# Optimization experiments

Measured on AMD Instinct MI355X. Metric: run time of the kernel, lower is better.

The kernel has to match this reference:

```python
import jax, jax.numpy as jnp
import numpy as np

N = 20000        # number of graph nodes (objects + regions)
E = 660000       # number of directed edges (~avg degree 33)
F_DIM = 254      # feature_dims = in_feats // 2
IN_FEATS = 508   # (256 - 2) * 2
GLOVE = 300


def _gcn_layer(x, W, b, src, dst, norm_src, norm_dst):
    """DGL GraphConv, norm='both'. W: [in, out], b: [out]."""
    n = x.shape[0]
    pre_mult = W.shape[0] > W.shape[1]  # DGL applies W first if in > out
    if pre_mult:
        x = x @ W
    h = (x * norm_src[:, None])[src]                      # [E, F] gather
    agg = jax.ops.segment_sum(h, dst, num_segments=n)     # scatter-add [N, F]
    agg = agg * norm_dst[:, None]
    if not pre_mult:
        agg = agg @ W
    return agg + b


def setup_inputs() -> dict:
    key = jax.random.key(0)
    ks = jax.random.split(key, 12)
    w = lambda k, shape: jax.random.normal(k, shape, jnp.float32) * 0.02
    return {
        "class_embed": jax.random.normal(ks[0], (N,), jnp.float32),
        "all_glove": jax.random.normal(ks[1], (N, GLOVE), jnp.float32),
        "W_word": w(ks[2], (F_DIM, GLOVE)),
        "b_word": jnp.zeros((F_DIM,), jnp.float32),
        "W_img": w(ks[3], (F_DIM, N)),
        "b_img": jnp.zeros((F_DIM,), jnp.float32),
        "W1": w(ks[4], (IN_FEATS, IN_FEATS)),
        "b1": jnp.zeros((IN_FEATS,), jnp.float32),
        "W2": w(ks[5], (IN_FEATS, IN_FEATS)),
        "b2": jnp.zeros((IN_FEATS,), jnp.float32),
        "W3": w(ks[6], (IN_FEATS, 1)),
        "b3": jnp.zeros((1,), jnp.float32),
        "W_fin": w(ks[7], (F_DIM, N)),
        "b_fin": jnp.zeros((F_DIM,), jnp.float32),
        "src": jax.random.randint(ks[8], (E,), 0, N, jnp.int32),
        "dst": jax.random.randint(ks[9], (E,), 0, N, jnp.int32),
    }


def reference(class_embed, all_glove, W_word, b_word, W_img, b_img,
              W1, b1, W2, b2, W3, b3, W_fin, b_fin, src, dst):
    n = all_glove.shape[0]
    ones = jnp.ones(src.shape, jnp.float32)
    deg_out = jax.ops.segment_sum(ones, src, num_segments=n)
    deg_in = jax.ops.segment_sum(ones, dst, num_segments=n)
    # norm='both': zero where degree is zero (DGL replaces inf with 0)
    norm_src = jnp.where(deg_out > 0, jnp.maximum(deg_out, 1.0) ** -0.5, 0.0)
    norm_dst = jnp.where(deg_in > 0, jnp.maximum(deg_in, 1.0) ** -0.5, 0.0)

    ce = class_embed.reshape(1, -1) @ W_img.T + b_img      # [1, 254]
    we = all_glove @ W_word.T + b_word                     # [N, 254]
    x = jnp.concatenate([jnp.broadcast_to(ce, (n, F_DIM)), we], axis=1)  # [N, 508]

    h = jax.nn.relu(_gcn_layer(x, W1, b1, src, dst, norm_src, norm_dst))
    h = jax.nn.relu(_gcn_layer(h, W2, b2, src, dst, norm_src, norm_dst))
    o = jax.nn.relu(_gcn_layer(h, W3, b3, src, dst, norm_src, norm_dst))  # [N, 1]

    return o.reshape(1, -1) @ W_fin.T + b_fin              # [1, 254]
```

## Files before the change

### kernel.cpp

```cpp
#include <hip/hip_runtime.h>
#include <hip/hip_bf16.h>

#define TPB 256
#define NB_E 32
#define HTPB 512
#define NHALF_LDS 10240

typedef __attribute__((ext_vector_type(8))) short bf16x8_t;
typedef __attribute__((ext_vector_type(4))) float f32x4_t;
typedef __attribute__((ext_vector_type(8))) unsigned short u16x8_t;
typedef __attribute__((ext_vector_type(4))) unsigned short u16x4_t;

__device__ __forceinline__ float bf2f(unsigned short u) {
    return __uint_as_float(((unsigned)u) << 16);
}
__device__ __forceinline__ unsigned short f2bf(float f) {
    unsigned x = __float_as_uint(f);
    unsigned r = (x + 0x7fff + ((x >> 16) & 1)) >> 16;
    return (unsigned short)r;
}

__device__ __forceinline__ void gload16(const unsigned short* g, unsigned short* l) {
    __builtin_amdgcn_global_load_lds(
        (const __attribute__((address_space(1))) unsigned int*)(const void*)g,
        (__attribute__((address_space(3))) unsigned int*)(void*)l, 16, 0, 0);
}


__global__ __launch_bounds__(HTPB) void hist_kernel(
    const int* __restrict__ src, const int* __restrict__ dst,
    int* __restrict__ histD, int* __restrict__ histS,
    int E, int N, int nhalf, int chunk) {
    __shared__ int h[NHALF_LDS];
    int b = blockIdx.x, var = blockIdx.y;
    const int* arr = (var < 2) ? dst : src;
    int lo = (var & 1) * nhalf;
    int hi = min(lo + nhalf, N);
    int cnt = hi - lo;
    for (int i = threadIdx.x; i < cnt; i += HTPB) h[i] = 0;
    __syncthreads();
    int beg = b * chunk, end = min(E, beg + chunk);
    for (int i = beg + threadIdx.x; i < end; i += HTPB) {
        int v = arr[i];
        if (v >= lo && v < hi) atomicAdd(&h[v - lo], 1);
    }
    __syncthreads();
    int* out = ((var < 2) ? histD : histS) + (size_t)b * N + lo;
    for (int i = threadIdx.x; i < cnt; i += HTPB) out[i] = h[i];
}

__global__ void degreduce_kernel(const int* __restrict__ histD, const int* __restrict__ histS,
                                 float* __restrict__ ns, float* __restrict__ nd,
                                 int* __restrict__ degp, int N) {
    int n = blockIdx.x * blockDim.x + threadIdx.x;
    if (n >= N) return;
    int di = 0, dout = 0;
    for (int b = 0; b < NB_E; b++) {
        di += histD[(size_t)b * N + n];
        dout += histS[(size_t)b * N + n];
    }
    nd[n] = di > 0 ? rsqrtf((float)di) : 0.f;
    ns[n] = dout > 0 ? rsqrtf((float)dout) : 0.f;
    degp[n] = (di + 7) & ~7;
}

__global__ __launch_bounds__(1024) void scan1(const int* __restrict__ degp,
                                              int* __restrict__ rp, int* __restrict__ bsum, int n) {
    __shared__ int buf[1024];
    int b = blockIdx.x;
    int i = b * 1024 + threadIdx.x;
    int v = (i < n) ? degp[i] : 0;
    buf[threadIdx.x] = v;
    __syncthreads();
    for (int off = 1; off < 1024; off <<= 1) {
        int t = (threadIdx.x >= off) ? buf[threadIdx.x - off] : 0;
        __syncthreads();
        buf[threadIdx.x] += t;
        __syncthreads();
    }
    if (i < n) rp[i + 1] = buf[threadIdx.x];
    if (threadIdx.x == 1023) bsum[b] = buf[1023];
    if (b == 0 && threadIdx.x == 0) rp[0] = 0;
}

__global__ void scan2(int* __restrict__ bsum, int nb) {
    int lane = threadIdx.x;
    int v = (lane < nb) ? bsum[lane] : 0;
    for (int off = 1; off < 64; off <<= 1) {
        int t = __shfl_up(v, off);
        if (lane >= off) v += t;
    }
    if (lane < nb) bsum[lane] = v;
}

__global__ __launch_bounds__(1024) void scan3(int* __restrict__ rp, const int* __restrict__ bsum, int n) {
    int b = blockIdx.x;
    if (b == 0) return;
    int i = b * 1024 + threadIdx.x;
    if (i < n) rp[i + 1] += bsum[b - 1];
}

__global__ void gbase_kernel(const int* __restrict__ histD, const int* __restrict__ rp,
                             int* __restrict__ gbase, int N) {
    int n = blockIdx.x * blockDim.x + threadIdx.x;
    if (n >= N) return;
    int run = rp[n];
    for (int b = 0; b < NB_E; b++) {
        gbase[(size_t)b * N + n] = run;
        run += histD[(size_t)b * N + n];
    }
}

__global__ __launch_bounds__(HTPB) void scatter2_kernel(
    const int* __restrict__ src, const int* __restrict__ dst,
    const int* __restrict__ gbase, const float* __restrict__ ns,
    int2* __restrict__ payload, int E, int N, int nhalf, int chunk) {
    __shared__ int h[NHALF_LDS];
    int b = blockIdx.x, half = blockIdx.y;
    int lo = half * nhalf;
    int hi = min(lo + nhalf, N);
    int cnt = hi - lo;
    for (int i = threadIdx.x; i < cnt; i += HTPB) h[i] = 0;
    __syncthreads();
    int beg = b * chunk, end = min(E, beg + chunk);
    for (int i = beg + threadIdx.x; i < end; i += HTPB) {
        int d = dst[i];
        if (d >= lo && d < hi) {
            int s = src[i];
            int rank = atomicAdd(&h[d - lo], 1);
            int pos = gbase[(size_t)b * N + d] + rank;
            payload[pos] = make_int2(s, __float_as_int(ns[s]));
        }
    }
}

__global__ __launch_bounds__(256) void st_kernel(const int* __restrict__ rp,
                                                 const int2* __restrict__ payload,
                                                 const float* __restrict__ nd,
                                                 float* __restrict__ tv, int n) {
    int d = blockIdx.x * 4 + (threadIdx.x >> 6);
    if (d >= n) return;
    int lane = threadIdx.x & 63;
    int beg = rp[d], end = rp[d + 1];
    float acc = 0.f;
    for (int e = beg + lane; e < end; e += 64) acc += __int_as_float(payload[e].y);
    for (int off = 32; off > 0; off >>= 1) acc += __shfl_down(acc, off);
    if (lane == 0) tv[d] = acc * nd[d];
}


__global__ void gemv_rows(const float* __restrict__ vec, const float* __restrict__ Mat,
                          const float* __restrict__ bias, float* __restrict__ out, int n) {
    int j = blockIdx.x;
    const float* row = Mat + (size_t)j * n;
    float s = 0.f;
    for (int i = threadIdx.x; i < n; i += blockDim.x) s += vec[i] * row[i];
    __shared__ float red[TPB];
    red[threadIdx.x] = s;
    __syncthreads();
    for (int o = TPB / 2; o > 0; o >>= 1) {
        if (threadIdx.x < o) red[threadIdx.x] += red[threadIdx.x + o];
        __syncthreads();
    }
    if (threadIdx.x == 0) out[j] = red[0] + (bias ? bias[j] : 0.f);
}

__global__ __launch_bounds__(64) void u_kernel(const float* __restrict__ ce, const float* __restrict__ W1,
                                               float* __restrict__ u, int FD, int IF) {
    int j = blockIdx.x;
    int lane = threadIdx.x;
    float s = 0.f;
    for (int i = lane; i < FD; i += 64) s += ce[i] * W1[(size_t)i * IF + j];
    for (int off = 32; off > 0; off >>= 1) s += __shfl_down(s, off);
    if (lane == 0) u[j] = s;
}


__global__ void pad_convert4(const float* __restrict__ in, int icols, int irows,
                             unsigned short* __restrict__ out, int ocols, int orows, int cpr) {
    int idx = blockIdx.x * blockDim.x + threadIdx.x;
    int row = idx / cpr;
    int c4 = (idx - row * cpr) * 4;
    if (row >= orows) return;
    float4 v = make_float4(0.f, 0.f, 0.f, 0.f);
    if (row < irows && c4 < icols)
        v = *(const float4*)(in + (size_t)row * icols + c4);
    u16x4_t o;
    o[0] = f2bf(v.x); o[1] = f2bf(v.y); o[2] = f2bf(v.z); o[3] = f2bf(v.w);
    *(u16x4_t*)(out + (size_t)row * ocols + c4) = o;
}

__global__ void transpose_pad(const float* __restrict__ W, int rows, int cols, int ldw,
                              unsigned short* __restrict__ out, int orows, int ocols) {
    __shared__ float tile[32][33];
    int k0 = blockIdx.x * 32, n0 = blockIdx.y * 32;
    int tx = threadIdx.x, ty = threadIdx.y;
    for (int i = 0; i < 32; i += 8) {
        int k = k0 + ty + i, n = n0 + tx;
        tile[ty + i][tx] = (k < rows && n < cols) ? W[(size_t)k * ldw + n] : 0.f;
    }
    __syncthreads();
    for (int i = 0; i < 32; i += 8) {
        int n = n0 + ty + i, k = k0 + tx;
        if (n < orows && k < ocols) out[(size_t)n * ocols + k] = f2bf(tile[tx][ty + i]);
    }
}

__global__ __launch_bounds__(256) void mfma_gemm(
    const unsigned short* __restrict__ A, const unsigned short* __restrict__ Bt,
    const float* __restrict__ bias, const float* __restrict__ rowscale,
    const float* __restrict__ tvec, const float* __restrict__ uvec,
    const float* __restrict__ w3, float* __restrict__ zout,
    unsigned short* __restrict__ C, int M, int Nn, int Kp, int Cld, int relu) {
    __shared__ unsigned short As[2][128 * 32];
    __shared__ unsigned short Bs[2][128 * 32];
    int tid = threadIdx.x;
    int lane = tid & 63;
    int wave = tid >> 6;
    int wm = wave >> 1, wn = wave & 1;
    int lg = lane >> 4, lt = lane & 15;

    int nwg = gridDim.x * gridDim.y;
    int hid = blockIdx.y * gridDim.x + blockIdx.x;
    int q = nwg >> 3, r8 = nwg & 7;
    int xcd = hid & 7, pos = hid >> 3;
    int wg = (xcd < r8 ? xcd * (q + 1) : r8 * (q + 1) + (xcd - r8) * q) + pos;
    int row0 = (wg / gridDim.x) * 128, col0 = (wg % gridDim.x) * 128;

    f32x4_t acc[4][4] = {};

    auto stage = [&](int b, int k0) {
#pragma unroll
        for (int i = 0; i < 2; i++) {
            int cid = tid + i * 256;
            int r = cid >> 2, c = cid & 3;
            int sw = c ^ ((r >> 1) & 3);
            gload16(A + (size_t)(row0 + r) * Kp + k0 + (sw << 3), As[b] + cid * 8);
            gload16(Bt + (size_t)(col0 + r) * Kp + k0 + (sw << 3), Bs[b] + cid * 8);
        }
    };

    int nk = Kp >> 5;
    stage(0, 0);
    __syncthreads();

    int cur = 0;
    for (int kp = 0; kp < nk; kp++) {
        if (kp + 1 < nk) stage(cur ^ 1, (kp + 1) << 5);
        bf16x8_t af[4], bfr[4];
#pragma unroll
        for (int mi = 0; mi < 4; mi++) {
            int r = wm * 64 + mi * 16 + lt;
            int sw = lg ^ ((r >> 1) & 3);
            af[mi] = *(const bf16x8_t*)(As[cur] + r * 32 + sw * 8);
        }
#pragma unroll
        for (int ni = 0; ni < 4; ni++) {
            int r = wn * 64 + ni * 16 + lt;
            int sw = lg ^ ((r >> 1) & 3);
            bfr[ni] = *(const bf16x8_t*)(Bs[cur] + r * 32 + sw * 8);
        }
#pragma unroll
        for (int mi = 0; mi < 4; mi++)
#pragma unroll
            for (int ni = 0; ni < 4; ni++)
                acc[mi][ni] = __builtin_amdgcn_mfma_f32_16x16x32_bf16(af[mi], bfr[ni], acc[mi][ni], 0, 0, 0);
        __syncthreads();
        cur ^= 1;
    }

#pragma unroll
    for (int mi = 0; mi < 4; mi++) {
#pragma unroll
        for (int r = 0; r < 4; r++) {
            int row = row0 + wm * 64 + mi * 16 + lg * 4 + r;
            if (row >= M) continue;
            float rs = rowscale ? rowscale[row] : 1.f;
            float tvr = tvec ? tvec[row] : 0.f;
            float zp = 0.f;
#pragma unroll
            for (int ni = 0; ni < 4; ni++) {
                int colb = col0 + wn * 64 + ni * 16 + lt;
                float v = 0.f;
                if (colb < Nn) {
                    v = acc[mi][ni][r] * rs;
                    if (bias) v += bias[colb];
                    if (tvec) v += tvr * uvec[colb];
                    if (relu) v = fmaxf(v, 0.f);
                    if (w3) zp += v * w3[colb];
                }
                if (C) C[(size_t)row * Cld + colb] = f2bf(v);
            }
            if (w3) {
                zp += __shfl_xor(zp, 1);
                zp += __shfl_xor(zp, 2);
                zp += __shfl_xor(zp, 4);
                zp += __shfl_xor(zp, 8);
                if (lt == 0) atomicAdd(&zout[row], zp);
            }
        }
    }
}

__global__ __launch_bounds__(256) void spmm_bf16_cols(
    const int* __restrict__ rp, const int2* __restrict__ payload,
    const unsigned short* __restrict__ X, unsigned short* __restrict__ Y,
    int n, int ld, int c0) {
    int node = blockIdx.x * 4 + (threadIdx.x >> 6);
    if (node >= n) return;
    int lane = threadIdx.x & 63;
    const unsigned short* Xo = X + c0 + lane * 4;
    int beg = rp[node], end = rp[node + 1];
    float acc[4] = {};
    for (int e = beg; e < end; e += 8) {
        int2 p[8];
#pragma unroll
        for (int j = 0; j < 8; j++) p[j] = payload[e + j];
        u16x4_t v[8];
#pragma unroll
        for (int j = 0; j < 8; j++) v[j] = *(const u16x4_t*)(Xo + (size_t)p[j].x * ld);
#pragma unroll
        for (int j = 0; j < 8; j++) {
            float w = __int_as_float(p[j].y);
#pragma unroll
            for (int c = 0; c < 4; c++) acc[c] += w * bf2f(v[j][c]);
        }
    }
    u16x4_t o;
#pragma unroll
    for (int c = 0; c < 4; c++) o[c] = f2bf(acc[c]);
    *(u16x4_t*)(Y + (size_t)node * ld + c0 + lane * 4) = o;
}


__global__ __launch_bounds__(256) void z_gather(const int* __restrict__ rp,
                                                const int2* __restrict__ payload,
                                                const float* __restrict__ z,
                                                const float* __restrict__ nd, const float* __restrict__ b3,
                                                float* __restrict__ o, int n) {
    int d = blockIdx.x * 4 + (threadIdx.x >> 6);
    if (d >= n) return;
    int lane = threadIdx.x & 63;
    int beg = rp[d], end = rp[d + 1];
    float acc = 0.f;
    for (int e = beg + lane; e < end; e += 64) {
        int2 p = payload[e];
        acc += __int_as_float(p.y) * z[p.x];
    }
    for (int off = 32; off > 0; off >>= 1) acc += __shfl_down(acc, off);
    if (lane == 0) o[d] = fmaxf(nd[d] * acc + b3[0], 0.f);
}


extern "C" void kernel_launch(void* const* d_in, const int* in_sizes, int n_in,
                              void* d_out, int out_size, void* d_ws, size_t ws_size,
                              hipStream_t stream) {
    const float* class_embed = (const float*)d_in[0];
    const float* all_glove   = (const float*)d_in[1];
    const float* W_word = (const float*)d_in[2];
    const float* b_word = (const float*)d_in[3];
    const float* W_img  = (const float*)d_in[4];
    const float* b_img  = (const float*)d_in[5];
    const float* W1 = (const float*)d_in[6];
    const float* b1 = (const float*)d_in[7];
    const float* W2 = (const float*)d_in[8];
    const float* b2 = (const float*)d_in[9];
    const float* W3 = (const float*)d_in[10];
    const float* b3 = (const float*)d_in[11];
    const float* W_fin = (const float*)d_in[12];
    const float* b_fin = (const float*)d_in[13];
    const int* src = (const int*)d_in[14];
    const int* dst = (const int*)d_in[15];

    const int N   = in_sizes[0];
    const int GLV = in_sizes[1] / N;
    const int FD  = in_sizes[5];
    const int IF  = in_sizes[7];
    const int E   = in_sizes[14];

    const int GLVp = 320;
    const int FDp  = 256;
    const int IFp  = 512;
    const int Mp   = (N + 127) & ~127;
    const int EP   = E + 8 * N;
    const int nhalf = (N + 1) / 2;
    const int chunk = (E + NB_E - 1) / NB_E;

    char* base = (char*)d_ws;
    size_t off = 0;
    auto alloc = [&](size_t bytes) -> void* {
        void* p = base + off;
        off = (off + bytes + 255) & ~(size_t)255;
        return p;
    };

    float* ns  = (float*)alloc((size_t)N * 4);
    float* nd  = (float*)alloc((size_t)N * 4);
    float* z   = (float*)alloc((size_t)N * 4);
    float* tv  = (float*)alloc((size_t)N * 4);
    float* ce  = (float*)alloc((size_t)FD * 4);
    float* u   = (float*)alloc((size_t)IF * 4);
    float* ov  = (float*)alloc((size_t)N * 4);
    int* degp  = (int*)alloc((size_t)N * 4);
    int* rp    = (int*)alloc((size_t)(N + 1) * 4);
    int* bsum  = (int*)alloc(64 * 4);
    int* histD = (int*)alloc((size_t)NB_E * N * 4);
    int* histS = (int*)alloc((size_t)NB_E * N * 4);
    int* gbase = (int*)alloc((size_t)NB_E * N * 4);
    int2* payload = (int2*)alloc((size_t)EP * 8);
    unsigned short* WwP  = (unsigned short*)alloc((size_t)FDp * GLVp * 2);
    unsigned short* W1hT = (unsigned short*)alloc((size_t)IFp * FDp * 2);
    unsigned short* W2T  = (unsigned short*)alloc((size_t)IFp * IFp * 2);
    unsigned short* glove_bf = (unsigned short*)alloc((size_t)Mp * GLVp * 2);
    unsigned short* we       = (unsigned short*)alloc((size_t)Mp * FDp * 2);
    unsigned short* h12      = (unsigned short*)alloc((size_t)Mp * IFp * 2);
    unsigned short* aggwe = glove_bf;
    unsigned short* agg2  = glove_bf;
    unsigned short* h1 = h12;

    hipMemsetAsync(z, 0, (size_t)N * 4, stream);
    hipMemsetAsync(payload, 0, (size_t)EP * 8, stream);

    int gN = (N + TPB - 1) / TPB;
    int nb = (N + 1023) / 1024;

    {
        dim3 g(NB_E, 4);
        hist_kernel<<<g, HTPB, 0, stream>>>(src, dst, histD, histS, E, N, nhalf, chunk);
    }
    degreduce_kernel<<<gN, TPB, 0, stream>>>(histD, histS, ns, nd, degp, N);
    scan1<<<nb, 1024, 0, stream>>>(degp, rp, bsum, N);
    scan2<<<1, 64, 0, stream>>>(bsum, nb);
    scan3<<<nb, 1024, 0, stream>>>(rp, bsum, N);
    gbase_kernel<<<gN, TPB, 0, stream>>>(histD, rp, gbase, N);
    {
        dim3 g(NB_E, 2);
        scatter2_kernel<<<g, HTPB, 0, stream>>>(src, dst, gbase, ns, payload, E, N, nhalf, chunk);
    }
    st_kernel<<<(N + 3) / 4, 256, 0, stream>>>(rp, payload, nd, tv, N);

    gemv_rows<<<FD, TPB, 0, stream>>>(class_embed, W_img, b_img, ce, N);
    u_kernel<<<IF, 64, 0, stream>>>(ce, W1, u, FD, IF);

    {
        int cpr = GLVp / 4;
        int tot = Mp * cpr;
        pad_convert4<<<(tot + 255) / 256, 256, 0, stream>>>(all_glove, GLV, N, glove_bf, GLVp, Mp, cpr);
        int tot2 = FDp * cpr;
        pad_convert4<<<(tot2 + 255) / 256, 256, 0, stream>>>(W_word, GLV, FD, WwP, GLVp, FDp, cpr);
    }
    {
        dim3 g(FDp / 32, IFp / 32);
        transpose_pad<<<g, dim3(32, 8), 0, stream>>>(W1 + (size_t)FD * IF, FD, IF, IF, W1hT, IFp, FDp);
    }
    {
        dim3 g(IFp / 32, IFp / 32);
        transpose_pad<<<g, dim3(32, 8), 0, stream>>>(W2, IF, IF, IF, W2T, IFp, IFp);
    }

    int mtiles = Mp / 128;

    {
        dim3 g(FDp / 128, mtiles);
        mfma_gemm<<<g, 256, 0, stream>>>(glove_bf, WwP, b_word, nullptr, nullptr, nullptr,
                                         nullptr, nullptr, we, N, FD, GLVp, FDp, 0);
    }
    spmm_bf16_cols<<<(N + 3) / 4, 256, 0, stream>>>(rp, payload, we, aggwe, N, FDp, 0);
    {
        dim3 g(IFp / 128, mtiles);
        mfma_gemm<<<g, 256, 0, stream>>>(aggwe, W1hT, b1, nd, tv, u,
                                         nullptr, nullptr, h1, N, IF, FDp, IFp, 1);
    }
    spmm_bf16_cols<<<(N + 3) / 4, 256, 0, stream>>>(rp, payload, h1, agg2, N, IFp, 0);
    spmm_bf16_cols<<<(N + 3) / 4, 256, 0, stream>>>(rp, payload, h1, agg2, N, IFp, 256);
    {
        dim3 g(IFp / 128, mtiles);
        mfma_gemm<<<g, 256, 0, stream>>>(agg2, W2T, b2, nd, nullptr, nullptr,
                                         W3, z, nullptr, N, IF, IFp, IFp, 1);
    }
    z_gather<<<(N + 3) / 4, 256, 0, stream>>>(rp, payload, z, nd, b3, ov, N);
    gemv_rows<<<FD, TPB, 0, stream>>>(ov, W_fin, b_fin, (float*)d_out, N);
}
```

Before: 369.9 us.

## Shrink GEMM tiles to 64x64 and split GEMV rows across slices with atomics

The MFMA GEMM tile drops from 128x128 to 64x64 (each wave now computes 2x2 MFMA blocks), which quadruples the number of workgroups so the 20000-row problem fills more CUs. The two GEMV kernels over N=20000 are each split into 8 slices per output row, combined with atomicAdd, and the output and ce buffers are zeroed by memsets. Smaller tiles give less operand reuse per workgroup and more global traffic, and the atomics make the summation order nondeterministic.

```diff
diff --git a/kernel.cpp b/kernel.cpp
--- a/kernel.cpp
+++ b/kernel.cpp
@@ -149,12 +149,15 @@
 }
 
 
-__global__ void gemv_rows(const float* __restrict__ vec, const float* __restrict__ Mat,
-                          const float* __restrict__ bias, float* __restrict__ out, int n) {
-    int j = blockIdx.x;
+__global__ void gemv_rows_split(const float* __restrict__ vec, const float* __restrict__ Mat,
+                                const float* __restrict__ bias, float* __restrict__ out,
+                                int n, int nslices) {
+    int j = blockIdx.x, slice = blockIdx.y;
+    int len = (n + nslices - 1) / nslices;
+    int beg = slice * len, end = min(n, beg + len);
     const float* row = Mat + (size_t)j * n;
     float s = 0.f;
-    for (int i = threadIdx.x; i < n; i += blockDim.x) s += vec[i] * row[i];
+    for (int i = beg + threadIdx.x; i < end; i += blockDim.x) s += vec[i] * row[i];
     __shared__ float red[TPB];
     red[threadIdx.x] = s;
     __syncthreads();
@@ -162,7 +165,10 @@
         if (threadIdx.x < o) red[threadIdx.x] += red[threadIdx.x + o];
         __syncthreads();
     }
-    if (threadIdx.x == 0) out[j] = red[0] + (bias ? bias[j] : 0.f);
+    if (threadIdx.x == 0) {
+        float v = red[0] + ((slice == 0 && bias) ? bias[j] : 0.f);
+        atomicAdd(&out[j], v);
+    }
 }
 
 __global__ __launch_bounds__(64) void u_kernel(const float* __restrict__ ce, const float* __restrict__ W1,
@@ -212,8 +218,8 @@
     const float* __restrict__ tvec, const float* __restrict__ uvec,
     const float* __restrict__ w3, float* __restrict__ zout,
     unsigned short* __restrict__ C, int M, int Nn, int Kp, int Cld, int relu) {
-    __shared__ unsigned short As[2][128 * 32];
-    __shared__ unsigned short Bs[2][128 * 32];
+    __shared__ unsigned short As[2][64 * 32];
+    __shared__ unsigned short Bs[2][64 * 32];
     int tid = threadIdx.x;
     int lane = tid & 63;
     int wave = tid >> 6;
@@ -225,62 +231,61 @@
     int q = nwg >> 3, r8 = nwg & 7;
     int xcd = hid & 7, pos = hid >> 3;
     int wg = (xcd < r8 ? xcd * (q + 1) : r8 * (q + 1) + (xcd - r8) * q) + pos;
-    int row0 = (wg / gridDim.x) * 128, col0 = (wg % gridDim.x) * 128;
-
-    f32x4_t acc[4][4] = {};
-
-    auto stage = [&](int b, int k0) {
-#pragma unroll
-        for (int i = 0; i < 2; i++) {
-            int cid = tid + i * 256;
-            int r = cid >> 2, c = cid & 3;
-            int sw = c ^ ((r >> 1) & 3);
-            gload16(A + (size_t)(row0 + r) * Kp + k0 + (sw << 3), As[b] + cid * 8);
-            gload16(Bt + (size_t)(col0 + r) * Kp + k0 + (sw << 3), Bs[b] + cid * 8);
-        }
-    };
+    int row0 = (wg / gridDim.x) * 64, col0 = (wg % gridDim.x) * 64;
+
+    f32x4_t acc[2][2] = {};
+
+    int sr = tid >> 2, sc = tid & 3;
+    int ssw = sc ^ ((sr >> 1) & 3);
+    const unsigned short* gA = A + (size_t)(row0 + sr) * Kp + (ssw << 3);
+    const unsigned short* gB = Bt + (size_t)(col0 + sr) * Kp + (ssw << 3);
 
     int nk = Kp >> 5;
-    stage(0, 0);
+    gload16(gA, As[0] + tid * 8);
+    gload16(gB, Bs[0] + tid * 8);
     __syncthreads();
 
     int cur = 0;
     for (int kp = 0; kp < nk; kp++) {
-        if (kp + 1 < nk) stage(cur ^ 1, (kp + 1) << 5);
-        bf16x8_t af[4], bfr[4];
-#pragma unroll
-        for (int mi = 0; mi < 4; mi++) {
-            int r = wm * 64 + mi * 16 + lt;
+        if (kp + 1 < nk) {
+            int k0 = (kp + 1) << 5;
+            gload16(gA + k0, As[cur ^ 1] + tid * 8);
+            gload16(gB + k0, Bs[cur ^ 1] + tid * 8);
+        }
+        bf16x8_t af[2], bfr[2];
+#pragma unroll
+        for (int mi = 0; mi < 2; mi++) {
+            int r = wm * 32 + mi * 16 + lt;
             int sw = lg ^ ((r >> 1) & 3);
             af[mi] = *(const bf16x8_t*)(As[cur] + r * 32 + sw * 8);
         }
 #pragma unroll
-        for (int ni = 0; ni < 4; ni++) {
-            int r = wn * 64 + ni * 16 + lt;
+        for (int ni = 0; ni < 2; ni++) {
+            int r = wn * 32 + ni * 16 + lt;
             int sw = lg ^ ((r >> 1) & 3);
             bfr[ni] = *(const bf16x8_t*)(Bs[cur] + r * 32 + sw * 8);
         }
 #pragma unroll
-        for (int mi = 0; mi < 4; mi++)
-#pragma unroll
-            for (int ni = 0; ni < 4; ni++)
+        for (int mi = 0; mi < 2; mi++)
+#pragma unroll
+            for (int ni = 0; ni < 2; ni++)
                 acc[mi][ni] = __builtin_amdgcn_mfma_f32_16x16x32_bf16(af[mi], bfr[ni], acc[mi][ni], 0, 0, 0);
         __syncthreads();
         cur ^= 1;
     }
 
 #pragma unroll
-    for (int mi = 0; mi < 4; mi++) {
+    for (int mi = 0; mi < 2; mi++) {
 #pragma unroll
         for (int r = 0; r < 4; r++) {
-            int row = row0 + wm * 64 + mi * 16 + lg * 4 + r;
+            int row = row0 + wm * 32 + mi * 16 + lg * 4 + r;
             if (row >= M) continue;
             float rs = rowscale ? rowscale[row] : 1.f;
             float tvr = tvec ? tvec[row] : 0.f;
             float zp = 0.f;
 #pragma unroll
-            for (int ni = 0; ni < 4; ni++) {
-                int colb = col0 + wn * 64 + ni * 16 + lt;
+            for (int ni = 0; ni < 2; ni++) {
+                int colb = col0 + wn * 32 + ni * 16 + lt;
                 float v = 0.f;
                 if (colb < Nn) {
                     v = acc[mi][ni][r] * rs;
@@ -381,7 +386,7 @@
     const int GLVp = 320;
     const int FDp  = 256;
     const int IFp  = 512;
-    const int Mp   = (N + 127) & ~127;
+    const int Mp   = (N + 63) & ~63;
     const int EP   = E + 8 * N;
     const int nhalf = (N + 1) / 2;
     const int chunk = (E + NB_E - 1) / NB_E;
@@ -394,11 +399,12 @@
         return p;
     };
 
+    float* z   = (float*)alloc((size_t)N * 4);
+    float* ce  = (float*)alloc((size_t)FD * 4);
+    size_t zero_bytes = (size_t)((char*)(ce + FD) - (char*)z);
     float* ns  = (float*)alloc((size_t)N * 4);
     float* nd  = (float*)alloc((size_t)N * 4);
-    float* z   = (float*)alloc((size_t)N * 4);
     float* tv  = (float*)alloc((size_t)N * 4);
-    float* ce  = (float*)alloc((size_t)FD * 4);
     float* u   = (float*)alloc((size_t)IF * 4);
     float* ov  = (float*)alloc((size_t)N * 4);
     int* degp  = (int*)alloc((size_t)N * 4);
@@ -418,8 +424,9 @@
     unsigned short* agg2  = glove_bf;
     unsigned short* h1 = h12;
 
-    hipMemsetAsync(z, 0, (size_t)N * 4, stream);
+    hipMemsetAsync(z, 0, zero_bytes, stream);
     hipMemsetAsync(payload, 0, (size_t)EP * 8, stream);
+    hipMemsetAsync(d_out, 0, (size_t)FD * 4, stream);
 
     int gN = (N + TPB - 1) / TPB;
     int nb = (N + 1023) / 1024;
@@ -439,7 +446,10 @@
     }
     st_kernel<<<(N + 3) / 4, 256, 0, stream>>>(rp, payload, nd, tv, N);
 
-    gemv_rows<<<FD, TPB, 0, stream>>>(class_embed, W_img, b_img, ce, N);
+    {
+        dim3 g(FD, 8);
+        gemv_rows_split<<<g, TPB, 0, stream>>>(class_embed, W_img, b_img, ce, N, 8);
+    }
     u_kernel<<<IF, 64, 0, stream>>>(ce, W1, u, FD, IF);
 
     {
@@ -458,26 +468,29 @@
         transpose_pad<<<g, dim3(32, 8), 0, stream>>>(W2, IF, IF, IF, W2T, IFp, IFp);
     }
 
-    int mtiles = Mp / 128;
-
-    {
-        dim3 g(FDp / 128, mtiles);
+    int mtiles = Mp / 64;
+
+    {
+        dim3 g(FDp / 64, mtiles);
         mfma_gemm<<<g, 256, 0, stream>>>(glove_bf, WwP, b_word, nullptr, nullptr, nullptr,
                                          nullptr, nullptr, we, N, FD, GLVp, FDp, 0);
     }
     spmm_bf16_cols<<<(N + 3) / 4, 256, 0, stream>>>(rp, payload, we, aggwe, N, FDp, 0);
     {
-        dim3 g(IFp / 128, mtiles);
+        dim3 g(IFp / 64, mtiles);
         mfma_gemm<<<g, 256, 0, stream>>>(aggwe, W1hT, b1, nd, tv, u,
                                          nullptr, nullptr, h1, N, IF, FDp, IFp, 1);
     }
     spmm_bf16_cols<<<(N + 3) / 4, 256, 0, stream>>>(rp, payload, h1, agg2, N, IFp, 0);
     spmm_bf16_cols<<<(N + 3) / 4, 256, 0, stream>>>(rp, payload, h1, agg2, N, IFp, 256);
     {
-        dim3 g(IFp / 128, mtiles);
+        dim3 g(IFp / 64, mtiles);
         mfma_gemm<<<g, 256, 0, stream>>>(agg2, W2T, b2, nd, nullptr, nullptr,
                                          W3, z, nullptr, N, IF, IFp, IFp, 1);
     }
     z_gather<<<(N + 3) / 4, 256, 0, stream>>>(rp, payload, z, nd, b3, ov, N);
-    gemv_rows<<<FD, TPB, 0, stream>>>(ov, W_fin, b_fin, (float*)d_out, N);
-}
+    {
+        dim3 g(FD, 8);
+        gemv_rows_split<<<g, TPB, 0, stream>>>(ov, W_fin, b_fin, (float*)d_out, N, 8);
+    }
+}
```

After: 327.4 us, median of 2. 1.13x faster.
